# Kernel optimization log

Hardware: AMD Instinct MI355X
Metric: run time of the kernel (lower is better)

## Reference

```python
import jax, jax.numpy as jnp
import numpy as np

N, E, NF, EF, G = 50000, 400000, 128, 64, 200


def _leaky(x):
    return jax.nn.leaky_relu(x, 0.01)


def _edge_softmax(logits, dst, n):
    # softmax over edges grouped by destination node; logits: [E, 1]
    m = jax.ops.segment_max(logits, dst, num_segments=n)
    m = jnp.where(jnp.isfinite(m), m, 0.0)  # guard empty segments
    e = jnp.exp(logits - m[dst])
    s = jax.ops.segment_sum(e, dst, num_segments=n)
    return e / s[dst]


def _gru(x, h, Wx, Wh, bx, bh):
    # torch.nn.GRUCell gate order: (r, z, n)
    gx = x @ Wx + bx
    gh = h @ Wh + bh
    H = h.shape[-1]
    r = jax.nn.sigmoid(gx[:, :H] + gh[:, :H])
    z = jax.nn.sigmoid(gx[:, H:2 * H] + gh[:, H:2 * H])
    nn_ = jnp.tanh(gx[:, 2 * H:] + r * gh[:, 2 * H:])
    return (1.0 - z) * nn_ + z * h


def setup_inputs() -> dict:
    key = jax.random.key(0)
    ks = jax.random.split(key, 20)
    f32 = jnp.float32
    w = lambda k, s: (jax.random.normal(k, s) * 0.05).astype(f32)
    z = lambda s: jnp.zeros(s, f32)
    return {
        "node_feats": jax.random.normal(ks[0], (N, NF), f32),
        "edge_feats": jax.random.normal(ks[1], (E, EF), f32),
        "gc_node_W": w(ks[4], (NF, G)), "gc_node_b": z((G,)),
        "gc_e1_W": w(ks[5], (NF + EF, G)), "gc_e1_b": z((G,)),
        "gc_e2_W": w(ks[6], (2 * G, 1)), "gc_e2_b": z((1,)),
        "gc_et_W": w(ks[7], (G, G)), "gc_et_b": z((G,)),
        "gc_gru_Wx": w(ks[8], (G, 3 * G)), "gc_gru_Wh": w(ks[9], (G, 3 * G)),
        "gc_gru_bx": z((3 * G,)), "gc_gru_bh": z((3 * G,)),
        "l1_e_W": w(ks[10], (2 * G, 1)), "l1_e_b": z((1,)),
        "l1_pn_W": w(ks[11], (G, G)), "l1_pn_b": z((G,)),
        "l1_gru_Wx": w(ks[12], (G, 3 * G)), "l1_gru_Wh": w(ks[13], (G, 3 * G)),
        "l1_gru_bx": z((3 * G,)), "l1_gru_bh": z((3 * G,)),
        "l1_bn_g": jnp.ones((G,), f32), "l1_bn_b": z((G,)),
        "src": jax.random.randint(ks[2], (E,), 0, N, jnp.int32),
        "dst": jax.random.randint(ks[3], (E,), 0, N, jnp.int32),
    }


def reference(node_feats, edge_feats,
              gc_node_W, gc_node_b, gc_e1_W, gc_e1_b, gc_e2_W, gc_e2_b,
              gc_et_W, gc_et_b, gc_gru_Wx, gc_gru_Wh, gc_gru_bx, gc_gru_bh,
              l1_e_W, l1_e_b, l1_pn_W, l1_pn_b, l1_gru_Wx, l1_gru_Wh,
              l1_gru_bx, l1_gru_bh, l1_bn_g, l1_bn_b, src, dst):
    n = node_feats.shape[0]
    # ---- GetContext ----
    hv_new = _leaky(node_feats @ gc_node_W + gc_node_b)                      # [N, G]
    he1 = _leaky(jnp.concatenate([node_feats[src], edge_feats], 1)
                 @ gc_e1_W + gc_e1_b)                                        # [E, G]
    logits = _leaky(jnp.concatenate([hv_new[dst], he1], 1)
                    @ gc_e2_W + gc_e2_b)                                     # [E, 1]
    a = _edge_softmax(logits, dst, n)
    e = a * (he1 @ gc_et_W + gc_et_b)
    c = jax.ops.segment_sum(e, dst, num_segments=n)                          # [N, G]
    h0 = jax.nn.relu(_gru(jax.nn.elu(c), hv_new,
                          gc_gru_Wx, gc_gru_Wh, gc_gru_bx, gc_gru_bh))
    # ---- GNNLayer ----
    logits2 = _leaky(jnp.concatenate([h0[dst], h0[src]], 1) @ l1_e_W + l1_e_b)
    a2 = _edge_softmax(logits2, dst, n) + 1.0
    hvp = h0 @ l1_pn_W + l1_pn_b
    c2 = jax.ops.segment_sum(hvp[src] * a2, dst, num_segments=n)
    h1 = jax.nn.relu(_gru(jax.nn.elu(c2), h0,
                          l1_gru_Wx, l1_gru_Wh, l1_gru_bx, l1_gru_bh))
    # BatchNorm1d (training-mode batch stats, eps=1e-5)
    mu = h1.mean(0)
    var = h1.var(0)
    h1 = l1_bn_g * (h1 - mu) / jnp.sqrt(var + 1e-5) + l1_bn_b
    return h0 + h1
```

## Files before the change

### kernel.cpp

```cpp
#include <hip/hip_runtime.h>
#include <math.h>

#define G 200
#define NF 128
#define EF 64

typedef __attribute__((ext_vector_type(8))) short bf16x8;
typedef __attribute__((ext_vector_type(4))) float f32x4;

__device__ __forceinline__ float leakyf(float x) { return x > 0.f ? x : 0.01f * x; }
__device__ __forceinline__ float eluf(float x)   { return x > 0.f ? x : (expf(x) - 1.f); }
__device__ __forceinline__ float sigm(float x)   { return 1.f / (1.f + expf(-x)); }

__device__ __forceinline__ unsigned short f2bf(float x) {
    union { float f; unsigned int u; } v; v.f = x;
    unsigned int r = v.u + 0x7FFF + ((v.u >> 16) & 1);
    return (unsigned short)(r >> 16);
}
__device__ __forceinline__ float bf2f(unsigned short u) {
    union { unsigned int i; float f; } v; v.i = ((unsigned int)u) << 16;
    return v.f;
}
__device__ __forceinline__ unsigned int pk2(float a, float b) {
    return (unsigned int)f2bf(a) | ((unsigned int)f2bf(b) << 16);
}

__global__ __launch_bounds__(256) void tprep_k(
    const float* __restrict__ W, unsigned short* __restrict__ Wt,
    int Kreal, int kpad, int Nstride, int Nreal)
{
    int total = 208 * kpad;
    for (int i = blockIdx.x * 256 + threadIdx.x; i < total; i += gridDim.x * 256) {
        int n = i / kpad, k = i % kpad;
        Wt[i] = (n < Nreal && k < Kreal) ? f2bf(W[(size_t)k * Nstride + n]) : 0;
    }
}

__global__ __launch_bounds__(256) void wgru3_k(
    const float* __restrict__ Wx, const float* __restrict__ Wh,
    unsigned short* __restrict__ Btrz, unsigned short* __restrict__ Btn)
{
    const int total = 512 * 416;
    for (int i = blockIdx.x * 256 + threadIdx.x; i < total; i += gridDim.x * 256) {
        int n = i / 416, k = i % 416;
        float v = 0.f;
        if (n < 416) {
            int gg = (n >= 208) ? 1 : 0;
            int c = n - gg * 208;
            if (c < 200) {
                if (k < 200)                  v = Wx[(size_t)k * 600 + gg * 200 + c];
                else if (k >= 208 && k < 408) v = Wh[(size_t)(k - 208) * 600 + gg * 200 + c];
            }
        }
        Btrz[i] = f2bf(v);

        float u = 0.f;
        int s = n >> 4, cc = n & 15;
        if (s < 26) {
            int c = (s >> 1) * 16 + cc;
            if (c < 200) {
                if (!(s & 1)) { if (k < 200) u = Wx[(size_t)k * 600 + 400 + c]; }
                else { if (k >= 208 && k < 408) u = Wh[(size_t)(k - 208) * 600 + 400 + c]; }
            }
        }
        Btn[i] = f2bf(u);
    }
}

__global__ __launch_bounds__(256) void gpack_k(
    const float* __restrict__ X, const float* __restrict__ H,
    unsigned short* __restrict__ Apk, int M, int Mpad)
{
    const long total = (long)Mpad * 52;
    for (long i = (long)blockIdx.x * 256 + threadIdx.x; i < total;
         i += (long)gridDim.x * 256) {
        int row = (int)(i / 52), ch = (int)(i % 52);
        uint4 u = make_uint4(0, 0, 0, 0);
        if (row < M) {
            if (ch < 25) {
                const float4* xp = (const float4*)(X + (size_t)row * 200 + ch * 8);
                float4 a = xp[0], b = xp[1];
                u.x = pk2(eluf(a.x), eluf(a.y)); u.y = pk2(eluf(a.z), eluf(a.w));
                u.z = pk2(eluf(b.x), eluf(b.y)); u.w = pk2(eluf(b.z), eluf(b.w));
            } else if (ch >= 26 && ch < 51) {
                const float4* hp = (const float4*)(H + (size_t)row * 200 + (ch - 26) * 8);
                float4 a = hp[0], b = hp[1];
                u.x = pk2(a.x, a.y); u.y = pk2(a.z, a.w);
                u.z = pk2(b.x, b.y); u.w = pk2(b.z, b.w);
            }
        }
        *(uint4*)&Apk[(size_t)row * 416 + ch * 8] = u;
    }
}

template <int EPI>
__global__ __launch_bounds__(256) void tgemm_k(
    const unsigned short* __restrict__ Apk,
    const unsigned short* __restrict__ Bt,
    const float* __restrict__ bx, const float* __restrict__ bh,
    unsigned short* __restrict__ RZ,
    float* __restrict__ OUT, int M)
{
    __shared__ __align__(16) unsigned short As[2][128 * 32];
    __shared__ __align__(16) unsigned short Bs[2][128 * 32];

    const int tid = threadIdx.x;
    const int w = tid >> 6, lane = tid & 63, l15 = lane & 15, lq = lane >> 4;
    const int wr = w >> 1, wc = w & 1;
    const int bm = blockIdx.x * 128, bn = blockIdx.y * 128;
    const int r0 = tid >> 2, sl = tid & 3;

    f32x4 acc[4][4];
#pragma unroll
    for (int a = 0; a < 4; ++a)
#pragma unroll
        for (int b = 0; b < 4; ++b) acc[a][b] = (f32x4){0.f, 0.f, 0.f, 0.f};

    {
        uint4 pa0 = *(const uint4*)&Apk[(size_t)(bm + r0) * 416 + sl * 8];
        uint4 pa1 = *(const uint4*)&Apk[(size_t)(bm + 64 + r0) * 416 + sl * 8];
        uint4 pb0 = *(const uint4*)&Bt[(size_t)(bn + r0) * 416 + sl * 8];
        uint4 pb1 = *(const uint4*)&Bt[(size_t)(bn + 64 + r0) * 416 + sl * 8];
        int w0 = sl ^ ((r0 >> 1) & 3), w1 = sl ^ (((r0 + 64) >> 1) & 3);
        *(uint4*)&As[0][r0 * 32 + w0 * 8] = pa0;
        *(uint4*)&As[0][(r0 + 64) * 32 + w1 * 8] = pa1;
        *(uint4*)&Bs[0][r0 * 32 + w0 * 8] = pb0;
        *(uint4*)&Bs[0][(r0 + 64) * 32 + w1 * 8] = pb1;
    }
    __syncthreads();

    int cur = 0;
    for (int c = 0; c < 13; ++c) {
        uint4 pa0, pa1, pb0, pb1;
        if (c < 12) {
            int kc = (c + 1) * 32;
            pa0 = *(const uint4*)&Apk[(size_t)(bm + r0) * 416 + kc + sl * 8];
            pa1 = *(const uint4*)&Apk[(size_t)(bm + 64 + r0) * 416 + kc + sl * 8];
            pb0 = *(const uint4*)&Bt[(size_t)(bn + r0) * 416 + kc + sl * 8];
            pb1 = *(const uint4*)&Bt[(size_t)(bn + 64 + r0) * 416 + kc + sl * 8];
        }
        bf16x8 af[4], bfr[4];
#pragma unroll
        for (int s = 0; s < 4; ++s) {
            int ra = wr * 64 + s * 16 + l15;
            af[s] = *(const bf16x8*)&As[cur][ra * 32 + (lq ^ ((ra >> 1) & 3)) * 8];
            int rb = wc * 64 + s * 16 + l15;
            bfr[s] = *(const bf16x8*)&Bs[cur][rb * 32 + (lq ^ ((rb >> 1) & 3)) * 8];
        }
#pragma unroll
        for (int sr = 0; sr < 4; ++sr)
#pragma unroll
            for (int sc = 0; sc < 4; ++sc)
                acc[sr][sc] = __builtin_amdgcn_mfma_f32_16x16x32_bf16(
                    af[sr], bfr[sc], acc[sr][sc], 0, 0, 0);

        if (c < 12) {
            int nb = cur ^ 1;
            int w0 = sl ^ ((r0 >> 1) & 3), w1 = sl ^ (((r0 + 64) >> 1) & 3);
            *(uint4*)&As[nb][r0 * 32 + w0 * 8] = pa0;
            *(uint4*)&As[nb][(r0 + 64) * 32 + w1 * 8] = pa1;
            *(uint4*)&Bs[nb][r0 * 32 + w0 * 8] = pb0;
            *(uint4*)&Bs[nb][(r0 + 64) * 32 + w1 * 8] = pb1;
        }
        __syncthreads();
        cur ^= 1;
    }

    if (EPI == 0) {
#pragma unroll
        for (int sr = 0; sr < 4; ++sr)
#pragma unroll
            for (int sc = 0; sc < 4; ++sc) {
                int col = bn + wc * 64 + sc * 16 + l15;
                if (col >= 416) continue;
                float bsum = (col < 208) ? (bx[col] + bh[col])
                                         : (bx[col - 8] + bh[col - 8]);
#pragma unroll
                for (int i = 0; i < 4; ++i) {
                    int row = bm + wr * 64 + sr * 16 + lq * 4 + i;
                    if (row < M)
                        RZ[(size_t)row * 416 + col] = f2bf(sigm(acc[sr][sc][i] + bsum));
                }
            }
    } else {
#pragma unroll
        for (int p = 0; p < 2; ++p) {
            int sglob = (bn >> 4) + wc * 4 + 2 * p;
            int cc = (sglob >> 1) * 16 + l15;
            if (cc >= 200) continue;
            float bxn = bx[400 + cc], bhn = bh[400 + cc];
#pragma unroll
            for (int sr = 0; sr < 4; ++sr)
#pragma unroll
                for (int i = 0; i < 4; ++i) {
                    int row = bm + wr * 64 + sr * 16 + lq * 4 + i;
                    if (row >= M) continue;
                    float rr = bf2f(RZ[(size_t)row * 416 + cc]);
                    float zz = bf2f(RZ[(size_t)row * 416 + 208 + cc]);
                    float hh = bf2f(Apk[(size_t)row * 416 + 208 + cc]);
                    float nn = tanhf(acc[sr][2 * p][i] + bxn +
                                     rr * (acc[sr][2 * p + 1][i] + bhn));
                    float o = (1.f - zz) * nn + zz * hh;
                    OUT[(size_t)row * 200 + cc] = fmaxf(o, 0.f);
                }
        }
    }
}

__global__ __launch_bounds__(256) void hist_k(
    const int* __restrict__ dst, int* __restrict__ cnt, int E)
{
    int i = blockIdx.x * 256 + threadIdx.x;
    if (i < E) atomicAdd(&cnt[dst[i]], 1);
}

__global__ __launch_bounds__(256) void scan_k(
    const int* __restrict__ cnt, int* __restrict__ offs,
    int* __restrict__ cursor, int Nn)
{
    __shared__ int wsum[4];
    const int tid = threadIdx.x;
    const int lane = tid & 63, wv = tid >> 6;
    int carry = 0;
    const int CH = 8;
    for (int base = 0; base < Nn; base += 256 * CH) {
        int v[CH]; int tsum = 0;
        int i0 = base + tid * CH;
#pragma unroll
        for (int j = 0; j < CH; ++j) {
            v[j] = (i0 + j < Nn) ? cnt[i0 + j] : 0;
            tsum += v[j];
        }
        int x = tsum;
        for (int off = 1; off < 64; off <<= 1) {
            int t = __shfl_up(x, off);
            if (lane >= off) x += t;
        }
        if (lane == 63) wsum[wv] = x;
        __syncthreads();
        int wbase = 0;
#pragma unroll
        for (int wq = 0; wq < 4; ++wq) wbase += (wq < wv) ? wsum[wq] : 0;
        int gtot = wsum[0] + wsum[1] + wsum[2] + wsum[3];
        int run = carry + wbase + (x - tsum);
#pragma unroll
        for (int j = 0; j < CH; ++j) {
            int idx = i0 + j;
            if (idx < Nn) { offs[idx] = run; cursor[idx] = run; }
            run += v[j];
        }
        carry += gtot;
        __syncthreads();
    }
    if (tid == 0) offs[Nn] = carry;
}

__global__ __launch_bounds__(256) void scatter_k(
    const int* __restrict__ src, const int* __restrict__ dst,
    int* __restrict__ cursor, int* __restrict__ eidC,
    int* __restrict__ srcC, int* __restrict__ dstC, int E)
{
    int i = blockIdx.x * 256 + threadIdx.x;
    if (i < E) {
        int d = dst[i];
        int pos = atomicAdd(&cursor[d], 1);
        eidC[pos] = i; srcC[pos] = src[i]; dstC[pos] = d;
    }
}

__global__ __launch_bounds__(256) void mgemm_k(
    const float* __restrict__ X, const unsigned short* __restrict__ Wt,
    const float* __restrict__ bias, float* __restrict__ OUT,
    int M, int Kreal, int kch, int astr, int leaky,
    const float* __restrict__ xdiv)
{
    __shared__ __align__(16) unsigned short A[64 * 232];
    const int tid = threadIdx.x;
    const int w = tid >> 6, lane = tid & 63, l15 = lane & 15, lq = lane >> 4;
    const int bm = blockIdx.x * 64;
    const int kpad = kch * 32;
    const int nch8 = Kreal >> 3;

    for (int i = tid; i < 64 * nch8; i += 256) {
        int r = i / nch8, ch = i % nch8;
        int grow = bm + r;
        uint4 u = make_uint4(0, 0, 0, 0);
        if (grow < M) {
            const float4* xp = (const float4*)(X + (size_t)grow * Kreal + ch * 8);
            float inv = 1.f;
            if (xdiv) { float dv = xdiv[grow]; inv = (dv > 0.f) ? 1.f / dv : 0.f; }
            float4 a = xp[0], b = xp[1];
            u.x = pk2(a.x * inv, a.y * inv); u.y = pk2(a.z * inv, a.w * inv);
            u.z = pk2(b.x * inv, b.y * inv); u.w = pk2(b.z * inv, b.w * inv);
        }
        *(uint4*)&A[r * astr + ch * 8] = u;
    }
    if (tid < 64) {
        for (int p = Kreal; p < kpad; p += 8)
            *(uint4*)&A[tid * astr + p] = make_uint4(0, 0, 0, 0);
    }
    __syncthreads();

    const int arow = (w * 16 + l15) * astr;
    f32x4 acc[13];
#pragma unroll
    for (int t = 0; t < 13; ++t) acc[t] = (f32x4){0.f, 0.f, 0.f, 0.f};

    for (int c = 0; c < kch; ++c) {
        bf16x8 a = *(const bf16x8*)&A[arow + c * 32 + lq * 8];
#pragma unroll
        for (int t = 0; t < 13; ++t) {
            bf16x8 b = *(const bf16x8*)&Wt[(size_t)(t * 16 + l15) * kpad + c * 32 + lq * 8];
            acc[t] = __builtin_amdgcn_mfma_f32_16x16x32_bf16(a, b, acc[t], 0, 0, 0);
        }
    }

    float rg[4];
#pragma unroll
    for (int i = 0; i < 4; ++i) {
        int grow = bm + w * 16 + lq * 4 + i;
        rg[i] = 1.f;
        if (xdiv && grow < M) rg[i] = (xdiv[grow] > 0.f) ? 1.f : 0.f;
    }

#pragma unroll
    for (int t = 0; t < 13; ++t) {
        int col = t * 16 + l15;
        if (col >= 200) continue;
        float bs = bias[col];
#pragma unroll
        for (int i = 0; i < 4; ++i) {
            int grow = bm + w * 16 + lq * 4 + i;
            if (grow >= M) continue;
            float v = acc[t][i] + bs * rg[i];
            OUT[(size_t)grow * 200 + col] = leaky ? leakyf(v) : v;
        }
    }
}

__global__ __launch_bounds__(256) void hd_k(
    const float* __restrict__ x, const float* __restrict__ W,
    float* __restrict__ hd, int Nn)
{
    int wid = blockIdx.x * 4 + (threadIdx.x >> 6);
    int lane = threadIdx.x & 63;
    if (wid >= Nn) return;
    float s = 0.f;
    for (int j = lane; j < G; j += 64) s += x[(size_t)wid * G + j] * W[j];
    for (int off = 32; off; off >>= 1) s += __shfl_down(s, off);
    if (lane == 0) hd[wid] = s;
}

__global__ __launch_bounds__(256) void edgefuse2_k(
    const float* __restrict__ node, const float* __restrict__ edgef,
    const int* __restrict__ srcC, const int* __restrict__ dstC,
    const int* __restrict__ eidC,
    const unsigned short* __restrict__ W1t, const float* __restrict__ b1,
    const float* __restrict__ e2W, const float* __restrict__ e2b,
    const float* __restrict__ hd,
    float* __restrict__ sden, float* __restrict__ hacc, int E)
{
    __shared__ __align__(16) unsigned short U[64 * 216];
    __shared__ __align__(16) unsigned short Wt[208 * 40];
    __shared__ float rowlg[64];
    __shared__ float pexp_s[64];
    __shared__ int   dst_s[64];

    const int tid  = threadIdx.x;
    const int w    = tid >> 6;
    const int lane = tid & 63;
    const int l15  = lane & 15;
    const int lq   = lane >> 4;
    const int eb   = blockIdx.x * 64;

    {
        const int r4 = tid >> 2, q = tid & 3;
        const int pos = eb + r4;
        if (pos < E) {
            const int se = srcC[pos];
            const int ei = eidC[pos];
            const float4* np = (const float4*)(node + (size_t)se * NF);
            const float4* ep = (const float4*)(edgef + (size_t)ei * EF);
            uint4* rowp = (uint4*)(U + r4 * 216);
#pragma unroll
            for (int i = 0; i < 4; ++i) {
                float4 a = np[q * 8 + 2 * i];
                float4 b = np[q * 8 + 2 * i + 1];
                uint4 u; u.x = pk2(a.x, a.y); u.y = pk2(a.z, a.w);
                u.z = pk2(b.x, b.y); u.w = pk2(b.z, b.w);
                rowp[q * 4 + i] = u;
            }
            uint4* edp = (uint4*)(U + r4 * 216 + 128);
#pragma unroll
            for (int i = 0; i < 2; ++i) {
                float4 a = ep[q * 4 + 2 * i];
                float4 b = ep[q * 4 + 2 * i + 1];
                uint4 u; u.x = pk2(a.x, a.y); u.y = pk2(a.z, a.w);
                u.z = pk2(b.x, b.y); u.w = pk2(b.z, b.w);
                edp[q * 2 + i] = u;
            }
        } else {
            uint4 z = make_uint4(0, 0, 0, 0);
            uint4* rowp = (uint4*)(U + r4 * 216);
#pragma unroll
            for (int i = 0; i < 4; ++i) rowp[q * 4 + i] = z;
            uint4* edp = (uint4*)(U + r4 * 216 + 128);
            edp[q * 2] = z; edp[q * 2 + 1] = z;
        }
        if (tid < 64) dst_s[tid] = (eb + tid < E) ? dstC[eb + tid] : -1;
    }
    __syncthreads();

    f32x4 acc[13];
#pragma unroll
    for (int t = 0; t < 13; ++t) acc[t] = (f32x4){0.f, 0.f, 0.f, 0.f};

    for (int c = 0; c < 6; ++c) {
        for (int q = tid; q < 832; q += 256) {
            int n = q >> 2, s = q & 3;
            *(uint4*)(Wt + n * 40 + s * 8) =
                *(const uint4*)(W1t + (size_t)n * 192 + c * 32 + s * 8);
        }
        __syncthreads();
        bf16x8 a = *(const bf16x8*)(U + (w * 16 + l15) * 216 + c * 32 + lq * 8);
#pragma unroll
        for (int t = 0; t < 13; ++t) {
            bf16x8 b = *(const bf16x8*)(Wt + (t * 16 + l15) * 40 + lq * 8);
            acc[t] = __builtin_amdgcn_mfma_f32_16x16x32_bf16(a, b, acc[t], 0, 0, 0);
        }
        __syncthreads();
    }

    float p[4] = {0.f, 0.f, 0.f, 0.f};
#pragma unroll
    for (int t = 0; t < 13; ++t) {
        const int col = t * 16 + l15;
#pragma unroll
        for (int r = 0; r < 4; ++r) {
            const int row = w * 16 + lq * 4 + r;
            float v = 0.f;
            if (col < 200) {
                v = leakyf(acc[t][r] + b1[col]);
                p[r] = fmaf(v, e2W[200 + col], p[r]);
            }
            U[row * 216 + col] = f2bf(v);
        }
    }
#pragma unroll
    for (int r = 0; r < 4; ++r) {
        p[r] += __shfl_xor(p[r], 1);
        p[r] += __shfl_xor(p[r], 2);
        p[r] += __shfl_xor(p[r], 4);
        p[r] += __shfl_xor(p[r], 8);
    }
    if (l15 == 0) {
#pragma unroll
        for (int r = 0; r < 4; ++r) rowlg[w * 16 + lq * 4 + r] = p[r];
    }
    __syncthreads();

    if (tid < 64) {
        float pe = 0.f;
        if (eb + tid < E) {
            float l = leakyf(rowlg[tid] + hd[dst_s[tid]] + e2b[0]);
            pe = expf(l);
            atomicAdd(&sden[dst_s[tid]], pe);
        }
        pexp_s[tid] = pe;
    }
    __syncthreads();

    if (tid < 200) {
        const int c = tid;
        float s = 0.f;
        int cur = dst_s[0];
        for (int r = 0; r < 64; ++r) {
            int d = dst_s[r];
            if (d < 0) break;
            if (d != cur) {
                atomicAdd(&hacc[(size_t)cur * 200 + c], s);
                s = 0.f; cur = d;
            }
            s = fmaf(pexp_s[r], bf2f(U[r * 216 + c]), s);
        }
        atomicAdd(&hacc[(size_t)cur * 200 + c], s);
    }
}

__global__ __launch_bounds__(256) void layer2b_k(
    const float* __restrict__ hvp,
    const float* __restrict__ hd2, const float* __restrict__ hs,
    const float* __restrict__ b,
    const int* __restrict__ offs, const int* __restrict__ srcC,
    float* __restrict__ c2, int Nn)
{
    const int wv = threadIdx.x >> 6;
    const int lane = threadIdx.x & 63;
    const int n = blockIdx.x * 4 + wv;
    if (n >= Nn) return;

    const int base = offs[n], end = offs[n + 1];
    const float hdn = hd2[n] + b[0];

    float ss = 0.f;
    for (int pos = base + lane; pos < end; pos += 64)
        ss += expf(leakyf(hdn + hs[srcC[pos]]));
    for (int off = 32; off; off >>= 1) ss += __shfl_xor(ss, off);
    float inv = (end > base) ? 1.f / ss : 0.f;

    float a0 = 0.f, a1 = 0.f, a2v = 0.f, a3 = 0.f;
    for (int pos = base; pos < end; ++pos) {
        int sidx = srcC[pos];
        float pe = expf(leakyf(hdn + hs[sidx]));
        float aw = pe * inv + 1.f;
        const float* vr = hvp + (size_t)sidx * 200;
        a0  += aw * vr[lane];
        a1  += aw * vr[64 + lane];
        a2v += aw * vr[128 + lane];
        if (lane < 8) a3 += aw * vr[192 + lane];
    }
    float* out = c2 + (size_t)n * 200;
    out[lane] = a0; out[64 + lane] = a1; out[128 + lane] = a2v;
    if (lane < 8) out[192 + lane] = a3;
}

__global__ __launch_bounds__(256) void bnstat2_k(
    const float* __restrict__ h1, float* __restrict__ stats, int Nn)
{
    const int c = threadIdx.x;
    if (c >= 200) return;
    float s = 0.f, s2 = 0.f;
    for (int r = blockIdx.x; r < Nn; r += gridDim.x) {
        float v = h1[(size_t)r * 200 + c];
        s += v; s2 += v * v;
    }
    atomicAdd(&stats[c], s);
    atomicAdd(&stats[G + c], s2);
}

__global__ __launch_bounds__(256) void final_k(
    float* __restrict__ out, const float* __restrict__ h1,
    const float* __restrict__ stats,
    const float* __restrict__ g, const float* __restrict__ bb, int Nn)
{
    long total = (long)Nn * G;
    for (long idx = (long)blockIdx.x * 256 + threadIdx.x; idx < total;
         idx += (long)gridDim.x * 256) {
        int c = (int)(idx % G);
        float mu  = stats[c] / Nn;
        float var = stats[G + c] / Nn - mu * mu;
        float xh  = (h1[idx] - mu) * rsqrtf(var + 1e-5f);
        out[idx] = out[idx] + g[c] * xh + bb[c];
    }
}

extern "C" void kernel_launch(void* const* d_in, const int* in_sizes, int n_in,
                              void* d_out, int out_size, void* d_ws, size_t ws_size,
                              hipStream_t stream)
{
    const float* node_feats = (const float*)d_in[0];
    const float* edge_feats = (const float*)d_in[1];
    const float* gc_node_W  = (const float*)d_in[2];
    const float* gc_node_b  = (const float*)d_in[3];
    const float* gc_e1_W    = (const float*)d_in[4];
    const float* gc_e1_b    = (const float*)d_in[5];
    const float* gc_e2_W    = (const float*)d_in[6];
    const float* gc_e2_b    = (const float*)d_in[7];
    const float* gc_et_W    = (const float*)d_in[8];
    const float* gc_et_b    = (const float*)d_in[9];
    const float* gc_gru_Wx  = (const float*)d_in[10];
    const float* gc_gru_Wh  = (const float*)d_in[11];
    const float* gc_gru_bx  = (const float*)d_in[12];
    const float* gc_gru_bh  = (const float*)d_in[13];
    const float* l1_e_W     = (const float*)d_in[14];
    const float* l1_e_b     = (const float*)d_in[15];
    const float* l1_pn_W    = (const float*)d_in[16];
    const float* l1_pn_b    = (const float*)d_in[17];
    const float* l1_gru_Wx  = (const float*)d_in[18];
    const float* l1_gru_Wh  = (const float*)d_in[19];
    const float* l1_gru_bx  = (const float*)d_in[20];
    const float* l1_gru_bh  = (const float*)d_in[21];
    const float* l1_bn_g    = (const float*)d_in[22];
    const float* l1_bn_b    = (const float*)d_in[23];
    const int*   src        = (const int*)d_in[24];
    const int*   dst        = (const int*)d_in[25];

    const int Nn = in_sizes[0] / NF;
    const int E  = in_sizes[24];
    const int Mpad = ((Nn + 127) / 128) * 128;

    float* ws = (float*)d_ws;
    size_t o = 0;
    float* hv    = ws + o; o += (size_t)Nn * G;
    float* cbuf  = ws + o; o += ((size_t)Mpad * 416 + 1) / 2;
    unsigned short* rzbuf = (unsigned short*)cbuf;
    float* sden  = ws + o; o += (size_t)Nn;
    float* hd    = ws + o; o += (size_t)Nn;
    float* hs    = ws + o; o += (size_t)Nn;
    float* stats = ws + o; o += 512;
    unsigned short* W1t_g  = (unsigned short*)(ws + o); o += (208 * 192) / 2;
    unsigned short* etWt_g = (unsigned short*)(ws + o); o += (208 * 224) / 2;
    unsigned short* ncWt_g = (unsigned short*)(ws + o); o += (208 * 128) / 2;
    unsigned short* pnWt_g = (unsigned short*)(ws + o); o += (208 * 224) / 2;
    unsigned short* Btrz1  = (unsigned short*)(ws + o); o += (512 * 416) / 2;
    unsigned short* Btn1   = (unsigned short*)(ws + o); o += (512 * 416) / 2;
    unsigned short* Btrz2  = (unsigned short*)(ws + o); o += (512 * 416) / 2;
    unsigned short* Btn2   = (unsigned short*)(ws + o); o += (512 * 416) / 2;
    int* cnt    = (int*)(ws + o); o += (size_t)Nn;
    int* offs   = (int*)(ws + o); o += (size_t)Nn + 1;
    int* cursor = (int*)(ws + o); o += (size_t)Nn;
    int* eidC   = (int*)(ws + o); o += (size_t)E;
    int* srcC   = (int*)(ws + o); o += (size_t)E;
    int* dstC   = (int*)(ws + o); o += (size_t)E;
    unsigned short* apack = (unsigned short*)(ws + o); o += ((size_t)Mpad * 416 + 1) / 2;

    float* h0  = (float*)d_out;
    float* hvp = hv;
    float* h1  = hv;

    const int gN64 = (Nn + 63) / 64;
    const int gE64 = (E + 63) / 64;
    const int gE256 = (E + 255) / 256;
    const int nWaves = (Nn + 3) / 4;
    const long totNG = (long)Nn * G;
    const dim3 gGEMM((Mpad / 128), 4);

    hipMemsetAsync(cnt, 0, (size_t)Nn * sizeof(int), stream);
    tprep_k<<<128, 256, 0, stream>>>(gc_e1_W,   W1t_g,  192, 192, 200, 200);
    tprep_k<<<128, 256, 0, stream>>>(gc_et_W,   etWt_g, 200, 224, 200, 200);
    tprep_k<<<128, 256, 0, stream>>>(gc_node_W, ncWt_g, 128, 128, 200, 200);
    tprep_k<<<128, 256, 0, stream>>>(l1_pn_W,   pnWt_g, 200, 224, 200, 200);
    wgru3_k<<<256, 256, 0, stream>>>(gc_gru_Wx, gc_gru_Wh, Btrz1, Btn1);
    wgru3_k<<<256, 256, 0, stream>>>(l1_gru_Wx, l1_gru_Wh, Btrz2, Btn2);
    hist_k<<<gE256, 256, 0, stream>>>(dst, cnt, E);
    scan_k<<<1, 256, 0, stream>>>(cnt, offs, cursor, Nn);
    scatter_k<<<gE256, 256, 0, stream>>>(src, dst, cursor, eidC, srcC, dstC, E);

    hipMemsetAsync(sden, 0, (size_t)Nn * sizeof(float), stream);
    hipMemsetAsync(cbuf, 0, (size_t)Nn * G * sizeof(float), stream);
    hipMemsetAsync(stats, 0, 512 * sizeof(float), stream);

    mgemm_k<<<gN64, 256, 0, stream>>>(node_feats, ncWt_g, gc_node_b, hv,
                                      Nn, 128, 4, 136, 1, nullptr);
    hd_k<<<nWaves, 256, 0, stream>>>(hv, gc_e2_W, hd, Nn);

    edgefuse2_k<<<gE64, 256, 0, stream>>>(
        node_feats, edge_feats, srcC, dstC, eidC,
        W1t_g, gc_e1_b, gc_e2_W, gc_e2_b, hd, sden, cbuf, E);

    mgemm_k<<<gN64, 256, 0, stream>>>(cbuf, etWt_g, gc_et_b, cbuf,
                                      Nn, 200, 7, 232, 0, sden);

    gpack_k<<<2048, 256, 0, stream>>>(cbuf, hv, apack, Nn, Mpad);
    tgemm_k<0><<<gGEMM, 256, 0, stream>>>(apack, Btrz1, gc_gru_bx, gc_gru_bh,
                                          rzbuf, nullptr, Nn);
    tgemm_k<1><<<gGEMM, 256, 0, stream>>>(apack, Btn1, gc_gru_bx, gc_gru_bh,
                                          rzbuf, h0, Nn);

    hd_k<<<nWaves, 256, 0, stream>>>(h0, l1_e_W, hd, Nn);
    hd_k<<<nWaves, 256, 0, stream>>>(h0, l1_e_W + 200, hs, Nn);

    mgemm_k<<<gN64, 256, 0, stream>>>(h0, pnWt_g, l1_pn_b, hvp,
                                      Nn, 200, 7, 232, 0, nullptr);

    layer2b_k<<<nWaves, 256, 0, stream>>>(hvp, hd, hs, l1_e_b,
                                          offs, srcC, cbuf, Nn);

    gpack_k<<<2048, 256, 0, stream>>>(cbuf, h0, apack, Nn, Mpad);
    tgemm_k<0><<<gGEMM, 256, 0, stream>>>(apack, Btrz2, l1_gru_bx, l1_gru_bh,
                                          rzbuf, nullptr, Nn);
    tgemm_k<1><<<gGEMM, 256, 0, stream>>>(apack, Btn2, l1_gru_bx, l1_gru_bh,
                                          rzbuf, h1, Nn);

    bnstat2_k<<<512, 256, 0, stream>>>(h1, stats, Nn);
    final_k<<<2048, 256, 0, stream>>>((float*)d_out, h1, stats,
                                      l1_bn_g, l1_bn_b, Nn);
}
```

Baseline: 1.020 ms.

## Fuse GRU input packing into producer epilogues and merge attention dot kernels

Removes the standalone gpack kernels. The bf16 packed GRU input is now written directly by the mgemm epilogues, by layer2b (with ELU applied) and by a new hdpair kernel, which also merges the two hd dot-product passes into one. The r/z gate buffer switches from bf16 to fp16, and the GRU n-epilogue reads the hidden state in fp32 from the original buffer. In exchange it adds a full memset of the packed buffer and scattered 2-byte writes in the epilogues.

```diff
diff --git a/kernel.cpp b/kernel.cpp
--- a/kernel.cpp
+++ b/kernel.cpp
@@ -67,38 +67,13 @@
     }
 }
 
-__global__ __launch_bounds__(256) void gpack_k(
-    const float* __restrict__ X, const float* __restrict__ H,
-    unsigned short* __restrict__ Apk, int M, int Mpad)
-{
-    const long total = (long)Mpad * 52;
-    for (long i = (long)blockIdx.x * 256 + threadIdx.x; i < total;
-         i += (long)gridDim.x * 256) {
-        int row = (int)(i / 52), ch = (int)(i % 52);
-        uint4 u = make_uint4(0, 0, 0, 0);
-        if (row < M) {
-            if (ch < 25) {
-                const float4* xp = (const float4*)(X + (size_t)row * 200 + ch * 8);
-                float4 a = xp[0], b = xp[1];
-                u.x = pk2(eluf(a.x), eluf(a.y)); u.y = pk2(eluf(a.z), eluf(a.w));
-                u.z = pk2(eluf(b.x), eluf(b.y)); u.w = pk2(eluf(b.z), eluf(b.w));
-            } else if (ch >= 26 && ch < 51) {
-                const float4* hp = (const float4*)(H + (size_t)row * 200 + (ch - 26) * 8);
-                float4 a = hp[0], b = hp[1];
-                u.x = pk2(a.x, a.y); u.y = pk2(a.z, a.w);
-                u.z = pk2(b.x, b.y); u.w = pk2(b.z, b.w);
-            }
-        }
-        *(uint4*)&Apk[(size_t)row * 416 + ch * 8] = u;
-    }
-}
-
 template <int EPI>
 __global__ __launch_bounds__(256) void tgemm_k(
     const unsigned short* __restrict__ Apk,
     const unsigned short* __restrict__ Bt,
     const float* __restrict__ bx, const float* __restrict__ bh,
-    unsigned short* __restrict__ RZ,
+    _Float16* __restrict__ RZ,
+    const float* __restrict__ Hf,
     float* __restrict__ OUT, int M)
 {
     __shared__ __align__(16) unsigned short As[2][128 * 32];
@@ -179,7 +154,8 @@
                 for (int i = 0; i < 4; ++i) {
                     int row = bm + wr * 64 + sr * 16 + lq * 4 + i;
                     if (row < M)
-                        RZ[(size_t)row * 416 + col] = f2bf(sigm(acc[sr][sc][i] + bsum));
+                        RZ[(size_t)row * 416 + col] =
+                            (_Float16)sigm(acc[sr][sc][i] + bsum);
                 }
             }
     } else {
@@ -195,9 +171,9 @@
                 for (int i = 0; i < 4; ++i) {
                     int row = bm + wr * 64 + sr * 16 + lq * 4 + i;
                     if (row >= M) continue;
-                    float rr = bf2f(RZ[(size_t)row * 416 + cc]);
-                    float zz = bf2f(RZ[(size_t)row * 416 + 208 + cc]);
-                    float hh = bf2f(Apk[(size_t)row * 416 + 208 + cc]);
+                    float rr = (float)RZ[(size_t)row * 416 + cc];
+                    float zz = (float)RZ[(size_t)row * 416 + 208 + cc];
+                    float hh = Hf[(size_t)row * 200 + cc];
                     float nn = tanhf(acc[sr][2 * p][i] + bxn +
                                      rr * (acc[sr][2 * p + 1][i] + bhn));
                     float o = (1.f - zz) * nn + zz * hh;
@@ -271,6 +247,7 @@
 __global__ __launch_bounds__(256) void mgemm_k(
     const float* __restrict__ X, const unsigned short* __restrict__ Wt,
     const float* __restrict__ bias, float* __restrict__ OUT,
+    unsigned short* __restrict__ APK, int amode,
     int M, int Kreal, int kch, int astr, int leaky,
     const float* __restrict__ xdiv)
 {
@@ -333,7 +310,15 @@
             int grow = bm + w * 16 + lq * 4 + i;
             if (grow >= M) continue;
             float v = acc[t][i] + bs * rg[i];
-            OUT[(size_t)grow * 200 + col] = leaky ? leakyf(v) : v;
+            if (amode == 0) {
+                OUT[(size_t)grow * 200 + col] = leaky ? leakyf(v) : v;
+            } else if (amode == 1) {
+                APK[(size_t)grow * 416 + col] = f2bf(eluf(v));
+            } else {
+                float lv = leakyf(v);
+                OUT[(size_t)grow * 200 + col] = lv;
+                APK[(size_t)grow * 416 + 208 + col] = f2bf(lv);
+            }
         }
     }
 }
@@ -349,6 +334,29 @@
     for (int j = lane; j < G; j += 64) s += x[(size_t)wid * G + j] * W[j];
     for (int off = 32; off; off >>= 1) s += __shfl_down(s, off);
     if (lane == 0) hd[wid] = s;
+}
+
+__global__ __launch_bounds__(256) void hdpair_k(
+    const float* __restrict__ x, const float* __restrict__ W,
+    float* __restrict__ hd2, float* __restrict__ hs,
+    unsigned short* __restrict__ APK, int Nn)
+{
+    int wid = blockIdx.x * 4 + (threadIdx.x >> 6);
+    int lane = threadIdx.x & 63;
+    if (wid >= Nn) return;
+    float s1 = 0.f, s2 = 0.f;
+    unsigned short* ap = APK + (size_t)wid * 416 + 208;
+    for (int j = lane; j < G; j += 64) {
+        float v = x[(size_t)wid * G + j];
+        s1 = fmaf(v, W[j], s1);
+        s2 = fmaf(v, W[200 + j], s2);
+        ap[j] = f2bf(v);
+    }
+    for (int off = 32; off; off >>= 1) {
+        s1 += __shfl_down(s1, off);
+        s2 += __shfl_down(s2, off);
+    }
+    if (lane == 0) { hd2[wid] = s1; hs[wid] = s2; }
 }
 
 __global__ __launch_bounds__(256) void edgefuse2_k(
@@ -492,7 +500,7 @@
     const float* __restrict__ hd2, const float* __restrict__ hs,
     const float* __restrict__ b,
     const int* __restrict__ offs, const int* __restrict__ srcC,
-    float* __restrict__ c2, int Nn)
+    unsigned short* __restrict__ APK, int Nn)
 {
     const int wv = threadIdx.x >> 6;
     const int lane = threadIdx.x & 63;
@@ -519,9 +527,11 @@
         a2v += aw * vr[128 + lane];
         if (lane < 8) a3 += aw * vr[192 + lane];
     }
-    float* out = c2 + (size_t)n * 200;
-    out[lane] = a0; out[64 + lane] = a1; out[128 + lane] = a2v;
-    if (lane < 8) out[192 + lane] = a3;
+    unsigned short* out = APK + (size_t)n * 416;
+    out[lane] = f2bf(eluf(a0));
+    out[64 + lane] = f2bf(eluf(a1));
+    out[128 + lane] = f2bf(eluf(a2v));
+    if (lane < 8) out[192 + lane] = f2bf(eluf(a3));
 }
 
 __global__ __launch_bounds__(256) void bnstat2_k(
@@ -593,7 +603,7 @@
     size_t o = 0;
     float* hv    = ws + o; o += (size_t)Nn * G;
     float* cbuf  = ws + o; o += ((size_t)Mpad * 416 + 1) / 2;
-    unsigned short* rzbuf = (unsigned short*)cbuf;
+    _Float16* rzbuf = (_Float16*)cbuf;
     float* sden  = ws + o; o += (size_t)Nn;
     float* hd    = ws + o; o += (size_t)Nn;
     float* hs    = ws + o; o += (size_t)Nn;
@@ -622,7 +632,6 @@
     const int gE64 = (E + 63) / 64;
     const int gE256 = (E + 255) / 256;
     const int nWaves = (Nn + 3) / 4;
-    const long totNG = (long)Nn * G;
     const dim3 gGEMM((Mpad / 128), 4);
 
     hipMemsetAsync(cnt, 0, (size_t)Nn * sizeof(int), stream);
@@ -639,38 +648,36 @@
     hipMemsetAsync(sden, 0, (size_t)Nn * sizeof(float), stream);
     hipMemsetAsync(cbuf, 0, (size_t)Nn * G * sizeof(float), stream);
     hipMemsetAsync(stats, 0, 512 * sizeof(float), stream);
+    hipMemsetAsync(apack, 0, (size_t)Mpad * 416 * sizeof(unsigned short), stream);
 
     mgemm_k<<<gN64, 256, 0, stream>>>(node_feats, ncWt_g, gc_node_b, hv,
-                                      Nn, 128, 4, 136, 1, nullptr);
+                                      apack, 2, Nn, 128, 4, 136, 1, nullptr);
     hd_k<<<nWaves, 256, 0, stream>>>(hv, gc_e2_W, hd, Nn);
 
     edgefuse2_k<<<gE64, 256, 0, stream>>>(
         node_feats, edge_feats, srcC, dstC, eidC,
         W1t_g, gc_e1_b, gc_e2_W, gc_e2_b, hd, sden, cbuf, E);
 
-    mgemm_k<<<gN64, 256, 0, stream>>>(cbuf, etWt_g, gc_et_b, cbuf,
-                                      Nn, 200, 7, 232, 0, sden);
-
-    gpack_k<<<2048, 256, 0, stream>>>(cbuf, hv, apack, Nn, Mpad);
+    mgemm_k<<<gN64, 256, 0, stream>>>(cbuf, etWt_g, gc_et_b, nullptr,
+                                      apack, 1, Nn, 200, 7, 232, 0, sden);
+
     tgemm_k<0><<<gGEMM, 256, 0, stream>>>(apack, Btrz1, gc_gru_bx, gc_gru_bh,
-                                          rzbuf, nullptr, Nn);
+                                          rzbuf, nullptr, nullptr, Nn);
     tgemm_k<1><<<gGEMM, 256, 0, stream>>>(apack, Btn1, gc_gru_bx, gc_gru_bh,
-                                          rzbuf, h0, Nn);
-
-    hd_k<<<nWaves, 256, 0, stream>>>(h0, l1_e_W, hd, Nn);
-    hd_k<<<nWaves, 256, 0, stream>>>(h0, l1_e_W + 200, hs, Nn);
+                                          rzbuf, hv, h0, Nn);
+
+    hdpair_k<<<nWaves, 256, 0, stream>>>(h0, l1_e_W, hd, hs, apack, Nn);
 
     mgemm_k<<<gN64, 256, 0, stream>>>(h0, pnWt_g, l1_pn_b, hvp,
-                                      Nn, 200, 7, 232, 0, nullptr);
+                                      nullptr, 0, Nn, 200, 7, 232, 0, nullptr);
 
     layer2b_k<<<nWaves, 256, 0, stream>>>(hvp, hd, hs, l1_e_b,
-                                          offs, srcC, cbuf, Nn);
-
-    gpack_k<<<2048, 256, 0, stream>>>(cbuf, h0, apack, Nn, Mpad);
+                                          offs, srcC, apack, Nn);
+
     tgemm_k<0><<<gGEMM, 256, 0, stream>>>(apack, Btrz2, l1_gru_bx, l1_gru_bh,
-                                          rzbuf, nullptr, Nn);
+                                          rzbuf, nullptr, nullptr, Nn);
     tgemm_k<1><<<gGEMM, 256, 0, stream>>>(apack, Btn2, l1_gru_bx, l1_gru_bh,
-                                          rzbuf, h1, Nn);
+                                          rzbuf, h0, h1, Nn);
 
     bnstat2_k<<<512, 256, 0, stream>>>(h1, stats, Nn);
     final_k<<<2048, 256, 0, stream>>>((float*)d_out, h1, stats,
```

New measurement: 986.8 us (median of 2 runs). 1.03x faster.
